# Optimization experiments

Hardware: AMD Instinct MI355X
Metric: run time of the kernel (lower is better)

Reference implementation:

```python
import jax, jax.numpy as jnp
import numpy as np
from jax import lax

HID = 256   # hidden_size
NN = 25     # n_nodes
T = 50      # seq_len
FIN = 16    # obs_length + 4
AS = 8      # action_space
HEADS = 5   # gat_head_num
E = 100     # edges per graph
B = 256     # batch


def setup_inputs() -> dict:
    key = jax.random.key(0)
    ks = jax.random.split(key, 32)
    s = 0.02
    def p(i, shape):
        return jax.random.normal(ks[i], shape, jnp.float32) * s
    return {
        "obs": jax.random.normal(ks[0], (B, NN, T, FIN), jnp.float32),
        "obs_map": jax.random.normal(ks[1], (B, 3, 84, 84), jnp.float32),
        "edges": jax.random.randint(ks[2], (B, 2, E), 0, NN),
        "edges_feature": jax.random.normal(ks[3], (B, E, 4), jnp.float32),
        "mlp_w": p(4, (FIN, HID)), "mlp_b": p(5, (HID,)),
        "c1_w": p(6, (32, 3, 8, 8)), "c1_b": p(7, (32,)),
        "c2_w": p(8, (64, 32, 4, 4)), "c2_b": p(9, (64,)),
        "c3_w": p(10, (64, 64, 3, 3)), "c3_b": p(11, (64,)),
        "fc_w": p(12, (3136, HID)), "fc_b": p(13, (HID,)),
        "gru_wih": p(14, (3 * HID, HID)), "gru_whh": p(15, (3 * HID, HID)),
        "gru_bih": p(16, (3 * HID,)), "gru_bhh": p(17, (3 * HID,)),
        "gat_wl": p(18, (HID, HEADS * HID)), "gat_bl": p(19, (HEADS * HID,)),
        "gat_wr": p(20, (HID, HEADS * HID)), "gat_br": p(21, (HEADS * HID,)),
        "gat_att": p(22, (HEADS, HID)), "gat_bias": p(23, (HID,)),
        "hid_w": p(24, (HID, HID)), "hid_b": p(25, (HID,)),
        "out_w": p(26, (HID, 1)), "out_b": p(27, (1,)),
        "adv_w": p(28, (HID, AS)), "adv_b": p(29, (AS,)),
    }


def _cnn(x, c1w, c1b, c2w, c2b, c3w, c3b, fcw, fcb):
    # Nature-CNN encoder: [B,3,84,84] -> [B,HID]
    dn = ('NCHW', 'OIHW', 'NCHW')
    h = jax.nn.relu(lax.conv_general_dilated(x, c1w, (4, 4), 'VALID', dimension_numbers=dn) + c1b[None, :, None, None])
    h = jax.nn.relu(lax.conv_general_dilated(h, c2w, (2, 2), 'VALID', dimension_numbers=dn) + c2b[None, :, None, None])
    h = jax.nn.relu(lax.conv_general_dilated(h, c3w, (1, 1), 'VALID', dimension_numbers=dn) + c3b[None, :, None, None])
    h = h.reshape(h.shape[0], -1)  # [B, 64*7*7]
    return jax.nn.relu(h @ fcw + fcb)


def _gru_last(x, wih, whh, bih, bhh):
    # torch nn.GRU (batch_first), return final hidden state [B,H]
    H = whh.shape[1]
    xg = x @ wih.T + bih  # precompute input gates [B,T,3H]
    def step(h, xg_t):
        hg = h @ whh.T + bhh
        xr, xz, xn = jnp.split(xg_t, 3, axis=-1)
        hr, hz, hn = jnp.split(hg, 3, axis=-1)
        r = jax.nn.sigmoid(xr + hr)
        z = jax.nn.sigmoid(xz + hz)
        n = jnp.tanh(xn + r * hn)
        return (1.0 - z) * n + z * h, None
    h0 = jnp.zeros((x.shape[0], H), x.dtype)
    hT, _ = lax.scan(step, h0, jnp.swapaxes(xg, 0, 1))
    return hT


def _gat(x, ei, wl, bl, wr, br, att, gbias):
    # GATv2Conv (concat=False): one graph, x [N,H], ei [2,E'] incl. self loops
    n = x.shape[0]
    heads, ch = att.shape
    src, dst = ei[0], ei[1]
    gl = (x @ wl + bl).reshape(n, heads, ch)
    gr = (x @ wr + br).reshape(n, heads, ch)
    e = jax.nn.leaky_relu(gl[src] + gr[dst], 0.2)          # [E',H,C]
    score = jnp.einsum('ehc,hc->eh', e, att)               # [E',H]
    m = jax.ops.segment_max(score, dst, num_segments=n)
    ex = jnp.exp(score - m[dst])
    den = jax.ops.segment_sum(ex, dst, num_segments=n)
    alpha = ex / den[dst]                                   # softmax per dst node
    out = jax.ops.segment_sum(alpha[:, :, None] * gl[src], dst, num_segments=n)
    return out.mean(axis=1) + gbias, alpha                  # mean over heads (concat=False)


def reference(obs, obs_map, edges, edges_feature, mlp_w, mlp_b, c1_w, c1_b, c2_w, c2_b, c3_w, c3_b, fc_w, fc_b, gru_wih, gru_whh, gru_bih, gru_bhh, gat_wl, gat_bl, gat_wr, gat_br, gat_att, gat_bias, hid_w, hid_b, out_w, out_b, adv_w, adv_b):
    bsz, n = obs.shape[0], obs.shape[1]
    n_edges = edges.shape[2]
    target_emb = _cnn(obs_map, c1_w, c1_b, c2_w, c2_b, c3_w, c3_b, fc_w, fc_b)[:, None, :]
    nbrs = obs[:, 1:].reshape(bsz * (n - 1), obs.shape[2], obs.shape[3])
    nbrs_emb = jax.nn.relu(nbrs @ mlp_w + mlp_b)            # MLP_rnn (Linear+ReLU)
    nbrs_h = _gru_last(nbrs_emb, gru_wih, gru_whh, gru_bih, gru_bhh).reshape(bsz, n - 1, -1)
    node_emb = jnp.concatenate([target_emb, nbrs_h], axis=1)  # [B,N,HID]
    loops = jnp.broadcast_to(jnp.arange(n)[None, None, :], (bsz, 2, n))
    ei = jnp.concatenate([edges, loops], axis=2)            # PyG add_self_loops (appended)
    gat_out, alpha = jax.vmap(lambda xg, eg: _gat(xg, eg, gat_wl, gat_bl, gat_wr, gat_br, gat_att, gat_bias))(node_emb, ei)
    att_w = alpha[:, : n_edges + 1].mean(axis=-1)           # matches att_weights[:-n_nodes+1].mean(axis=1)
    h = jax.nn.relu(gat_out[:, 0] @ hid_w + hid_b)          # only node-0 feature used
    v = h @ out_w + out_b
    adv = h @ adv_w + adv_b
    q = v + (adv - adv.mean(axis=-1, keepdims=True))        # dueling head
    return q, att_w
```

## Files before the change

### kernel.cpp

```cpp
#include <hip/hip_runtime.h>
#include <cstdint>

typedef __attribute__((ext_vector_type(8))) __bf16 bf16x8;
typedef __attribute__((ext_vector_type(4))) float f32x4;
typedef __attribute__((ext_vector_type(4))) unsigned int uint4v;
typedef __attribute__((ext_vector_type(2))) unsigned int uint2v;
typedef __attribute__((ext_vector_type(4))) float float4v;
typedef __attribute__((ext_vector_type(2))) long long2v;

__device__ __forceinline__ unsigned short f2bf(float x){
  union { float f; unsigned u; } v; v.f = x;
  unsigned r = v.u + 0x7FFFu + ((v.u >> 16) & 1u);
  return (unsigned short)(r >> 16);
}
__device__ __forceinline__ float bf2f(unsigned short h){
  union { unsigned u; float f; } v; v.u = ((unsigned)h) << 16;
  return v.f;
}
__device__ __forceinline__ float bflo(unsigned u){
  union { unsigned x; float f; } v; v.x = u << 16; return v.f;
}
__device__ __forceinline__ float bfhi(unsigned u){
  union { unsigned x; float f; } v; v.x = u & 0xFFFF0000u; return v.f;
}
__device__ __forceinline__ f32x4 MFMA16(bf16x8 a, bf16x8 b, f32x4 c){
  return __builtin_amdgcn_mfma_f32_16x16x32_bf16(a, b, c, 0, 0, 0);
}
__device__ __forceinline__ f32x4 MFMA8(long a, long b, f32x4 c){
  return __builtin_amdgcn_mfma_f32_16x16x32_fp8_fp8(a, b, c, 0, 0, 0);
}
__device__ __forceinline__ unsigned char f2fp8(float x){
  int p = __builtin_amdgcn_cvt_pk_fp8_f32(x, x, 0, false);
  return (unsigned char)(p & 0xFF);
}

__global__ __launch_bounds__(256) void prep_k(
    const float* __restrict__ wih, const float* __restrict__ whh,
    const float* __restrict__ bl, const float* __restrict__ br,
    const float* __restrict__ mlpw,
    const float* __restrict__ c2w, const float* __restrict__ c3w,
    const float* __restrict__ fcw, const float* __restrict__ wl, const float* __restrict__ wr,
    unsigned char* __restrict__ wfrag8, unsigned short* __restrict__ mlpfrag,
    float* __restrict__ blbr,
    unsigned short* __restrict__ c2wb, unsigned short* __restrict__ c3wb,
    unsigned short* __restrict__ fcwT, unsigned short* __restrict__ wlrT){
  __shared__ float tile[64][65];
  int bid = blockIdx.x, t = threadIdx.x;
  if (bid < 1850){
    int i = bid*256 + t;
    if (i < 393216){
      int b16 = i & 15;
      int l   = (i >> 4) & 63;
      int chunk = i >> 10;
      int wkp = chunk / 6;
      int mg  = chunk - 6*wkp;
      int w = wkp >> 2, kkp = wkp & 3;
      int ks = b16 >> 3, e = b16 & 7;
      int kk = kkp*2 + ks;
      int mat = mg / 3, g = mg - 3*(mg/3);
      int n = g*256 + w*16 + (l & 15);
      int k = kk*32 + (l >> 4)*8 + e;
      float v = 16.f * (mat ? whh[n*256 + k] : wih[n*256 + k]);
      wfrag8[i] = f2fp8(v);
      return;
    }
    i -= 393216;
    if (i < 8192){
      int w = i >> 9;
      int r4 = i & 511;
      int l = r4 >> 3, e = r4 & 7;
      int n = w*16 + (l & 15);
      int k = (l >> 4)*8 + e;
      mlpfrag[i] = (k < 16) ? f2bf(mlpw[k*256 + n]) : (unsigned short)0;
      return;
    }
    i -= 8192;
    if (i < 2560){
      blbr[i] = (i < 1280) ? bl[i] : br[i-1280];
      return;
    }
    i -= 2560;
    if (i < 32768){ c2wb[i] = f2bf(c2w[i]); return; }
    i -= 32768;
    if (i < 36864){ c3wb[i] = f2bf(c3w[i]); }
    return;
  }
  if (bid < 2046){
    int tb = bid - 1850;
    int ti = tb >> 2, tj = tb & 3;
    for (int idx = t; idx < 4096; idx += 256){
      int r = idx >> 6, c = idx & 63;
      tile[r][c] = fcw[(size_t)(ti*64 + r)*256 + tj*64 + c];
    }
    __syncthreads();
    for (int idx = t; idx < 4096; idx += 256){
      int r = idx >> 6, c = idx & 63;
      fcwT[(size_t)(tj*64 + r)*3136 + ti*64 + c] = f2bf(tile[c][r]);
    }
    return;
  }
  {
    int tb = bid - 2046;
    int m = tb / 80; int rem = tb - m*80;
    int tk = rem / 20, tn = rem - tk*20;
    const float* src = m ? wr : wl;
    for (int idx = t; idx < 4096; idx += 256){
      int r = idx >> 6, c = idx & 63;
      tile[r][c] = src[(size_t)(tk*64 + r)*1280 + tn*64 + c];
    }
    __syncthreads();
    for (int idx = t; idx < 4096; idx += 256){
      int r = idx >> 6, c = idx & 63;
      wlrT[(size_t)(m*1280 + tn*64 + r)*256 + tk*64 + c] = f2bf(tile[c][r]);
    }
  }
}

__global__ __launch_bounds__(1024) void conv23_k(const unsigned short* __restrict__ c1o,
              const unsigned short* __restrict__ c2wb, const float* __restrict__ c2b,
              const unsigned short* __restrict__ c3wb, const float* __restrict__ c3b,
              unsigned short* __restrict__ c3o){
  __shared__ __align__(16) char cs[102016];
  unsigned short* in_s = (unsigned short*)cs;
  unsigned short* w2s  = (unsigned short*)(cs + 25600);
  float* b2            = (float*)(cs + 91136);
  unsigned short* c2s  = (unsigned short*)(cs + 91392);
  unsigned short* w3s  = (unsigned short*)cs;
  float* b3            = (float*)(cs + 101760);
  int b = blockIdx.x, t = threadIdx.x;
  int q = t >> 8, t2 = t & 255;
  for (int idx = t; idx < 12800; idx += 1024) in_s[idx] = c1o[(size_t)b*12800 + idx];
  for (int idx = t; idx < 32768; idx += 1024) w2s[idx] = c2wb[idx];
  if (t < 64) b2[t] = c2b[t];
  if (t >= 64 && t < 128) b3[t-64] = c3b[t-64];
  __syncthreads();
  for (int p = t2; p < 432; p += 256){
    int ocl = p / 27; int rem = p - ocl*27;
    int oy = rem / 3, og = rem - oy*3;
    int oc = q*16 + ocl;
    float a0=b2[oc],a1=b2[oc],a2=b2[oc];
    #pragma unroll 4
    for (int ic=0;ic<32;ic++){
      #pragma unroll
      for (int ky=0;ky<4;ky++){
        const unsigned short* row = &in_s[(ic*20 + oy*2+ky)*20 + og*6];
        float s[8];
        #pragma unroll
        for (int cc=0;cc<8;cc++) s[cc]=bf2f(row[cc]);
        const unsigned short* wp = &w2s[((oc*32+ic)*4+ky)*4];
        #pragma unroll
        for (int kx=0;kx<4;kx++){
          float wv = bf2f(wp[kx]);
          a0 += s[kx]*wv; a1 += s[2+kx]*wv; a2 += s[4+kx]*wv;
        }
      }
    }
    int ob = (oc*9 + oy)*9 + og*3;
    c2s[ob+0]=f2bf(fmaxf(a0,0.f)); c2s[ob+1]=f2bf(fmaxf(a1,0.f)); c2s[ob+2]=f2bf(fmaxf(a2,0.f));
  }
  __syncthreads();
  for (int idx = t; idx < 36864; idx += 1024) w3s[idx] = c3wb[idx];
  __syncthreads();
  for (int p = t2; p < 224; p += 256){
    int ocl = p / 14; int rem = p - ocl*14;
    int oy = rem >> 1, og = rem & 1;
    int ox0 = og*4; int nx = og ? 3 : 4;
    int oc = q*16 + ocl;
    float a[4]; a[0]=a[1]=a[2]=a[3]=b3[oc];
    for (int ic=0;ic<64;ic++){
      #pragma unroll
      for (int ky=0;ky<3;ky++){
        const unsigned short* row = &c2s[(ic*9 + oy+ky)*9 + ox0];
        float s[6];
        #pragma unroll
        for (int cc=0;cc<6;cc++) s[cc] = (ox0+cc < 9) ? bf2f(row[cc]) : 0.f;
        const unsigned short* wp = &w3s[((oc*64+ic)*3+ky)*3];
        #pragma unroll
        for (int kx=0;kx<3;kx++){
          float wv = bf2f(wp[kx]);
          #pragma unroll
          for (int jj=0;jj<4;jj++) a[jj] += s[jj+kx]*wv;
        }
      }
    }
    size_t ob = (size_t)b*3136 + oc*49 + oy*7 + ox0;
    #pragma unroll
    for (int jj=0;jj<4;jj++) if (jj < nx) c3o[ob+jj] = f2bf(fmaxf(a[jj],0.f));
  }
}

__global__ __launch_bounds__(256) void gemm_k(const unsigned short* __restrict__ A,
              const unsigned short* __restrict__ B, const float* __restrict__ bias,
              unsigned short* __restrict__ C, int K, int ldc, int rowmul, int relu, int Nblk){
  __shared__ __align__(16) unsigned short As[64*32];
  __shared__ __align__(16) unsigned short Bs[64*32];
  int bid = blockIdx.x;
  int nb = bid % Nblk, mb = bid / Nblk;
  int t = threadIdx.x;
  int w = t >> 6, l = t & 63, lr = l & 15, lh = l >> 4;
  int sr = t >> 2, sq = t & 3;
  f32x4 acc[4];
  #pragma unroll
  for (int i=0;i<4;i++) acc[i] = (f32x4){0.f,0.f,0.f,0.f};
  int nkk = K >> 5;
  const size_t a_row = (size_t)(mb*64 + sr)*K;
  const size_t b_row = (size_t)(nb*64 + sr)*K;
  for (int kk=0;kk<nkk;kk++){
    uint4v av = *(const uint4v*)&A[a_row + kk*32 + sq*8];
    uint4v bv = *(const uint4v*)&B[b_row + kk*32 + sq*8];
    __syncthreads();
    *(uint4v*)((char*)As + ((sr*64 + sq*16) ^ ((sr&3)<<4))) = av;
    *(uint4v*)((char*)Bs + ((sr*64 + sq*16) ^ ((sr&3)<<4))) = bv;
    __syncthreads();
    int brow = w*16 + lr;
    bf16x8 bfr = *(const bf16x8*)((char*)Bs + ((brow*64 + lh*16) ^ ((brow&3)<<4)));
    #pragma unroll
    for (int mt=0;mt<4;mt++){
      int arow = mt*16 + lr;
      bf16x8 afr = *(const bf16x8*)((char*)As + ((arow*64 + lh*16) ^ ((arow&3)<<4)));
      acc[mt] = MFMA16(afr, bfr, acc[mt]);
    }
  }
  int col = nb*64 + w*16 + lr;
  float bn = bias[col];
  #pragma unroll
  for (int mt=0;mt<4;mt++){
    #pragma unroll
    for (int r=0;r<4;r++){
      int row = mb*64 + mt*16 + lh*4 + r;
      float v = acc[mt][r] + bn;
      if (relu) v = fmaxf(v, 0.f);
      C[(size_t)row*rowmul*ldc + col] = f2bf(v);
    }
  }
}

__global__ __launch_bounds__(256) void gemm_fc_k(const unsigned short* __restrict__ A,
              const unsigned short* __restrict__ B, float* __restrict__ P){
  __shared__ __align__(16) unsigned short As[64*32];
  __shared__ __align__(16) unsigned short Bs[64*32];
  int bid = blockIdx.x;
  int s = bid % 7, tile = bid / 7;
  int nb = tile & 3, mb = tile >> 2;
  int t = threadIdx.x;
  int w = t >> 6, l = t & 63, lr = l & 15, lh = l >> 4;
  int sr = t >> 2, sq = t & 3;
  f32x4 acc[4];
  #pragma unroll
  for (int i=0;i<4;i++) acc[i] = (f32x4){0.f,0.f,0.f,0.f};
  const int K = 3136;
  const size_t a_row = (size_t)(mb*64 + sr)*K;
  const size_t b_row = (size_t)(nb*64 + sr)*K;
  for (int kk = s*14; kk < s*14 + 14; kk++){
    uint4v av = *(const uint4v*)&A[a_row + kk*32 + sq*8];
    uint4v bv = *(const uint4v*)&B[b_row + kk*32 + sq*8];
    __syncthreads();
    *(uint4v*)((char*)As + ((sr*64 + sq*16) ^ ((sr&3)<<4))) = av;
    *(uint4v*)((char*)Bs + ((sr*64 + sq*16) ^ ((sr&3)<<4))) = bv;
    __syncthreads();
    int brow = w*16 + lr;
    bf16x8 bfr = *(const bf16x8*)((char*)Bs + ((brow*64 + lh*16) ^ ((brow&3)<<4)));
    #pragma unroll
    for (int mt=0;mt<4;mt++){
      int arow = mt*16 + lr;
      bf16x8 afr = *(const bf16x8*)((char*)As + ((arow*64 + lh*16) ^ ((arow&3)<<4)));
      acc[mt] = MFMA16(afr, bfr, acc[mt]);
    }
  }
  int col = nb*64 + w*16 + lr;
  #pragma unroll
  for (int mt=0;mt<4;mt++){
    #pragma unroll
    for (int r=0;r<4;r++){
      int row = mb*64 + mt*16 + lh*4 + r;
      P[(size_t)s*65536 + row*256 + col] = acc[mt][r];
    }
  }
}

__global__ __launch_bounds__(256) void fc_red_k(const float* __restrict__ P,
              const float* __restrict__ fcb, unsigned short* __restrict__ nemb){
  int idx = blockIdx.x*256 + threadIdx.x;
  int row = idx >> 8, col = idx & 255;
  float sum = fcb[col];
  #pragma unroll
  for (int k=0;k<7;k++) sum += P[k*65536 + idx];
  nemb[(size_t)row*25*256 + col] = f2bf(fmaxf(sum, 0.f));
}

__global__ __launch_bounds__(1024, 4)
void gruconv_k(const float* __restrict__ obs,
              const unsigned char* __restrict__ wfrag8,
              const unsigned short* __restrict__ mlpfrag,
              const float* __restrict__ mlpb,
              const float* __restrict__ bih, const float* __restrict__ bhh,
              unsigned short* __restrict__ nemb,
              const float* __restrict__ cin, const float* __restrict__ c1w,
              const float* __restrict__ c1b, unsigned short* __restrict__ c1o){
  __shared__ __align__(16) char smem[121984];

  const int t = threadIdx.x, blk = blockIdx.x;

  if (blk >= 192){
    float* in_s = (float*)smem;
    float* w_s  = (float*)(smem + 96768);
    float* b_s  = (float*)(smem + 121344);
    int b = blk - 192;
    int q = t >> 8, t2 = t & 255;
    float* inq = in_s + q*6048;
    for (int idx = t2; idx < 3*24*84; idx += 256){
      int ic = idx / (24*84); int rem = idx - ic*(24*84);
      int iy = rem / 84, ix = rem - iy*84;
      inq[idx] = cin[((size_t)(b*3+ic)*84 + (q*20 + iy))*84 + ix];
    }
    for (int idx = t; idx < 32*192; idx += 1024) w_s[idx] = c1w[idx];
    if (t < 32) b_s[t] = c1b[t];
    __syncthreads();
    for (int p = t2; p < 800; p += 256){
      int oc = p / 25; int rem = p - oc*25;
      int oy = rem / 5, og = rem - oy*5;
      float a0=b_s[oc],a1=b_s[oc],a2=b_s[oc],a3=b_s[oc];
      #pragma unroll
      for (int ic=0;ic<3;ic++){
        #pragma unroll
        for (int ky=0;ky<8;ky++){
          const float* row = &inq[(ic*24 + oy*4+ky)*84 + og*16];
          float s[20];
          #pragma unroll
          for (int cc=0;cc<20;cc++) s[cc]=row[cc];
          const float* wp = &w_s[(oc*3 + ic)*64 + ky*8];
          #pragma unroll
          for (int kx=0;kx<8;kx++){
            float wv = wp[kx];
            a0 += s[kx]*wv; a1 += s[4+kx]*wv; a2 += s[8+kx]*wv; a3 += s[12+kx]*wv;
          }
        }
      }
      size_t ob = ((size_t)(b*32+oc)*20 + (q*5+oy))*20 + og*4;
      c1o[ob+0]=f2bf(fmaxf(a0,0.f)); c1o[ob+1]=f2bf(fmaxf(a1,0.f));
      c1o[ob+2]=f2bf(fmaxf(a2,0.f)); c1o[ob+3]=f2bf(fmaxf(a3,0.f));
    }
    return;
  }

  unsigned short* obsA = (unsigned short*)smem;
  unsigned char* e8_0 = (unsigned char*)(smem + 2048);
  unsigned char* e8_1 = (unsigned char*)(smem + 10240);
  unsigned char* h8   = (unsigned char*)(smem + 18432);

  obsA[t & 1023] = 0;
  for (int j = t; j < 8192; j += 1024) h8[j] = 0;

  const int w = t >> 6, l = t & 63, lr = l & 15, lh = l >> 4;
  const int jcol = w*16 + lr;
  const float bR  = bih[jcol]     + bhh[jcol];
  const float bZ  = bih[256+jcol] + bhh[256+jcol];
  const float bXN = bih[512+jcol];
  const float bHN = bhh[512+jcol];
  const float bMb = mlpb[jcol];
  const bf16x8 bMLP = *(const bf16x8*)(mlpfrag + w*512 + l*8);

  const unsigned char* wb8 = wfrag8 + w*24576 + l*16;

  const int srow = t >> 2, sk4 = t & 3;
  int rrS = blk*32 + srow; int bS = rrS/24, ndS = 1 + (rrS - bS*24);
  const float* obase4 = obs + (size_t)(bS*25 + ndS)*800 + sk4*4;
  const int obyte = (srow*64 + sk4*8) ^ ((srow&3)<<4);

  const int a8off = lr*256 + lh*8;
  const int xr8 = lr << 3;
  const int o16 = lh*16;
  const int oa0b = (lr*64 + o16) ^ ((lr&3)<<4);
  const int oa1b = ((16+lr)*64 + o16) ^ ((lr&3)<<4);
  const int hw0 = jcol;
  const float S = 1.f/256.f;

  f32x4 hs0 = (f32x4){0.f,0.f,0.f,0.f};
  f32x4 hs1 = (f32x4){0.f,0.f,0.f,0.f};

#define EMB_COMPUTE(DST) { \
  f32x4 e0 = (f32x4){0.f,0.f,0.f,0.f}, e1 = (f32x4){0.f,0.f,0.f,0.f}; \
  bf16x8 oa0 = *(const bf16x8*)((char*)obsA + oa0b); \
  bf16x8 oa1 = *(const bf16x8*)((char*)obsA + oa1b); \
  e0 = MFMA16(oa0, bMLP, e0); \
  e1 = MFMA16(oa1, bMLP, e1); \
  _Pragma("unroll") \
  for (int r=0;r<4;r++){ \
    int m = lh*4 + r; \
    (DST)[(m*256 + hw0) ^ ((m&15)<<3)] = f2fp8(fmaxf(e0[r] + bMb, 0.f)*16.f); \
    int m2 = m + 16; \
    (DST)[(m2*256 + hw0) ^ ((m2&15)<<3)] = f2fp8(fmaxf(e1[r] + bMb, 0.f)*16.f); \
  } }

  __syncthreads();
  if (t < 128){
    float4v ov = *(const float4v*)(obase4);
    uint2v pk;
    pk[0] = (unsigned)f2bf(ov[0]) | ((unsigned)f2bf(ov[1]) << 16);
    pk[1] = (unsigned)f2bf(ov[2]) | ((unsigned)f2bf(ov[3]) << 16);
    *(uint2v*)((char*)obsA + obyte) = pk;
  }
  __syncthreads();
  EMB_COMPUTE(e8_0)
  __syncthreads();

  for (int step=0; step<50; step++){
    const unsigned char* ebuf = (step & 1) ? e8_1 : e8_0;
    unsigned char* nbuf = (step & 1) ? e8_0 : e8_1;
    const bool stg = (t < 128) && (step < 49);
    float4v ov;
    if (stg) ov = *(const float4v*)(obase4 + (size_t)(step+1)*16);

    f32x4 aR0=(f32x4){0,0,0,0}, aR1=(f32x4){0,0,0,0};
    f32x4 aZ0=(f32x4){0,0,0,0}, aZ1=(f32x4){0,0,0,0};
    f32x4 aN0=(f32x4){0,0,0,0}, aN1=(f32x4){0,0,0,0};
    f32x4 aM0=(f32x4){0,0,0,0}, aM1=(f32x4){0,0,0,0};
    __builtin_amdgcn_s_setprio(1);
    #pragma unroll 2
    for (int kkp=0;kkp<4;kkp++){
      const unsigned char* wk8 = wb8 + kkp*6144;
      long2v wIR = *(const long2v*)(wk8);
      long2v wIZ = *(const long2v*)(wk8 + 1024);
      long2v wIN = *(const long2v*)(wk8 + 2048);
      long2v wHR = *(const long2v*)(wk8 + 3072);
      long2v wHZ = *(const long2v*)(wk8 + 4096);
      long2v wHN = *(const long2v*)(wk8 + 5120);
      {
        int kk = kkp*2;
        int ab = a8off + kk*32;
        long eA0 = *(const long*)(ebuf + (ab ^ xr8));
        long eA1 = *(const long*)(ebuf + ((ab + 4096) ^ xr8));
        long hA0 = *(const long*)(h8 + (ab ^ xr8));
        long hA1 = *(const long*)(h8 + ((ab + 4096) ^ xr8));
        aR0 = MFMA8(eA0, wIR[0], aR0);  aR0 = MFMA8(hA0, wHR[0], aR0);
        aR1 = MFMA8(eA1, wIR[0], aR1);  aR1 = MFMA8(hA1, wHR[0], aR1);
        aZ0 = MFMA8(eA0, wIZ[0], aZ0);  aZ0 = MFMA8(hA0, wHZ[0], aZ0);
        aZ1 = MFMA8(eA1, wIZ[0], aZ1);  aZ1 = MFMA8(hA1, wHZ[0], aZ1);
        aN0 = MFMA8(eA0, wIN[0], aN0);  aN1 = MFMA8(eA1, wIN[0], aN1);
        aM0 = MFMA8(hA0, wHN[0], aM0);  aM1 = MFMA8(hA1, wHN[0], aM1);
      }
      {
        int kk = kkp*2 + 1;
        int ab = a8off + kk*32;
        long eA0 = *(const long*)(ebuf + (ab ^ xr8));
        long eA1 = *(const long*)(ebuf + ((ab + 4096) ^ xr8));
        long hA0 = *(const long*)(h8 + (ab ^ xr8));
        long hA1 = *(const long*)(h8 + ((ab + 4096) ^ xr8));
        aR0 = MFMA8(eA0, wIR[1], aR0);  aR0 = MFMA8(hA0, wHR[1], aR0);
        aR1 = MFMA8(eA1, wIR[1], aR1);  aR1 = MFMA8(hA1, wHR[1], aR1);
        aZ0 = MFMA8(eA0, wIZ[1], aZ0);  aZ0 = MFMA8(hA0, wHZ[1], aZ0);
        aZ1 = MFMA8(eA1, wIZ[1], aZ1);  aZ1 = MFMA8(hA1, wHZ[1], aZ1);
        aN0 = MFMA8(eA0, wIN[1], aN0);  aN1 = MFMA8(eA1, wIN[1], aN1);
        aM0 = MFMA8(hA0, wHN[1], aM0);  aM1 = MFMA8(hA1, wHN[1], aM1);
      }
    }
    __builtin_amdgcn_s_setprio(0);
    if (stg){
      uint2v pk;
      pk[0] = (unsigned)f2bf(ov[0]) | ((unsigned)f2bf(ov[1]) << 16);
      pk[1] = (unsigned)f2bf(ov[2]) | ((unsigned)f2bf(ov[3]) << 16);
      *(uint2v*)((char*)obsA + obyte) = pk;
    }
    __syncthreads();
    if (step < 49){
      EMB_COMPUTE(nbuf)
    }
    #pragma unroll
    for (int mt=0;mt<2;mt++){
      f32x4 vR = mt ? aR1 : aR0;
      f32x4 vZ = mt ? aZ1 : aZ0;
      f32x4 vN = mt ? aN1 : aN0;
      f32x4 vM = mt ? aM1 : aM0;
      #pragma unroll
      for (int r=0;r<4;r++){
        float rp = vR[r]*S + bR;
        float zp = vZ[r]*S + bZ;
        float xn = vN[r]*S + bXN;
        float hn = vM[r]*S + bHN;
        float rg = 1.f/(1.f + __expf(-rp));
        float zg = 1.f/(1.f + __expf(-zp));
        float arg = xn + rg*hn;
        float e2 = __expf(2.f*arg);
        float nv = (e2 - 1.f)/(e2 + 1.f);
        float hold = mt ? hs1[r] : hs0[r];
        float hnew = (1.f - zg)*nv + zg*hold;
        if (mt) hs1[r] = hnew; else hs0[r] = hnew;
        int m = mt*16 + lh*4 + r;
        h8[(m*256 + hw0) ^ ((m&15)<<3)] = f2fp8(hnew*16.f);
        if (step == 49){
          int rr = blk*32 + m; int b = rr/24; int nd = 1 + (rr - b*24);
          nemb[(size_t)(b*25+nd)*256 + jcol] = f2bf(hnew);
        }
      }
    }
    __syncthreads();
  }
#undef EMB_COMPUTE
}

__global__ __launch_bounds__(1024) void gat_k(const int* __restrict__ edges,
              const unsigned short* __restrict__ glgr,
              const float* __restrict__ att, const float* __restrict__ gbias,
              const float* __restrict__ hidw, const float* __restrict__ hidb,
              const float* __restrict__ outw, const float* __restrict__ outb,
              const float* __restrict__ advw, const float* __restrict__ advb,
              float* __restrict__ out){
  __shared__ int src_s[125], dst_s[125];
  __shared__ __align__(16) float att_s[1280];
  __shared__ float sc[125][5], al[125][5];
  __shared__ float mx[25][5], dn[25][5];
  __shared__ float g0p[4][256];
  __shared__ float hp[4][256];
  __shared__ float g0[256], hh[256];
  __shared__ float adv_s[8], v_s;
  __shared__ int e0[125]; __shared__ int ne0;

  int b = blockIdx.x, t = threadIdx.x;
  int qq = t >> 8, t2 = t & 255;
  if (t < 100){ src_s[t] = edges[b*200 + t]; dst_s[t] = edges[b*200 + 100 + t]; }
  else if (t < 125){ src_s[t] = t - 100; dst_s[t] = t - 100; }
  for (int j = t; j < 1280; j += 1024) att_s[j] = att[j];
  __syncthreads();
  if (t == 0){ int c = 0; for (int e=0;e<125;e++) if (dst_s[e]==0) e0[c++]=e; ne0 = c; }
  const unsigned short* gbase = glgr + (size_t)b*25*2560;
  if (t < 625){
    int e = t/5, h = t - 5*(t/5);
    const unsigned short* glp = gbase + src_s[e]*2560 + h*256;
    const unsigned short* grp = gbase + dst_s[e]*2560 + 1280 + h*256;
    const float* ap = &att_s[h*256];
    float acc = 0.f;
    #pragma unroll 4
    for (int c=0;c<256;c+=8){
      uint4v gu = *(const uint4v*)&glp[c];
      uint4v ru = *(const uint4v*)&grp[c];
      #pragma unroll
      for (int q=0;q<4;q++){
        float s0 = bflo(gu[q]) + bflo(ru[q]);
        float s1 = bfhi(gu[q]) + bfhi(ru[q]);
        s0 = (s0 > 0.f) ? s0 : 0.2f*s0;
        s1 = (s1 > 0.f) ? s1 : 0.2f*s1;
        acc += s0*ap[c+2*q] + s1*ap[c+2*q+1];
      }
    }
    sc[e][h] = acc;
  }
  __syncthreads();
  if (t < 125){
    int j = t/5, h = t - 5*(t/5);
    float m = -1e30f;
    for (int e=0;e<125;e++) if (dst_s[e]==j) m = fmaxf(m, sc[e][h]);
    float d = 0.f;
    for (int e=0;e<125;e++) if (dst_s[e]==j) d += __expf(sc[e][h]-m);
    mx[j][h] = m; dn[j][h] = d;
  }
  __syncthreads();
  if (t < 625){
    int e = t/5, h = t - 5*(t/5);
    int dd = dst_s[e];
    al[e][h] = __expf(sc[e][h] - mx[dd][h]) / dn[dd][h];
  }
  __syncthreads();
  if (t < 101){
    out[2048 + b*101 + t] = (al[t][0]+al[t][1]+al[t][2]+al[t][3]+al[t][4])*0.2f;
  }
  {
    float acc = 0.f;
    for (int x=qq; x<ne0; x+=4){
      int e = e0[x]; int s = src_s[e];
      const unsigned short* glp = gbase + s*2560 + t2;
      #pragma unroll
      for (int h=0;h<5;h++) acc += al[e][h]*bf2f(glp[h*256]);
    }
    g0p[qq][t2] = acc;
  }
  __syncthreads();
  if (t < 256){
    g0[t] = (g0p[0][t]+g0p[1][t]+g0p[2][t]+g0p[3][t])*0.2f + gbias[t];
  }
  __syncthreads();
  {
    float acc = 0.f;
    int k0 = qq*64;
    for (int k=k0;k<k0+64;k++) acc += g0[k]*hidw[k*256+t2];
    hp[qq][t2] = acc;
  }
  __syncthreads();
  if (t < 256){
    hh[t] = fmaxf(hidb[t] + hp[0][t]+hp[1][t]+hp[2][t]+hp[3][t], 0.f);
  }
  __syncthreads();
  if (t < 8){
    float acc = advb[t];
    for (int k=0;k<256;k++) acc += hh[k]*advw[k*8+t];
    adv_s[t] = acc;
  } else if (t == 8){
    float acc = outb[0];
    for (int k=0;k<256;k++) acc += hh[k]*outw[k];
    v_s = acc;
  }
  __syncthreads();
  if (t < 8){
    float m = adv_s[0]+adv_s[1]+adv_s[2]+adv_s[3]+adv_s[4]+adv_s[5]+adv_s[6]+adv_s[7];
    out[b*8+t] = v_s + adv_s[t] - m*0.125f;
  }
}

extern "C" void kernel_launch(void* const* d_in, const int* in_sizes, int n_in,
                              void* d_out, int out_size, void* d_ws, size_t ws_size,
                              hipStream_t stream){
  const float* obs     = (const float*)d_in[0];
  const float* obs_map = (const float*)d_in[1];
  const int*   edges   = (const int*)d_in[2];
  const float* mlp_w = (const float*)d_in[4];
  const float* mlp_b = (const float*)d_in[5];
  const float* c1w = (const float*)d_in[6];  const float* c1b = (const float*)d_in[7];
  const float* c2w = (const float*)d_in[8];  const float* c2b = (const float*)d_in[9];
  const float* c3w = (const float*)d_in[10]; const float* c3b = (const float*)d_in[11];
  const float* fcw = (const float*)d_in[12]; const float* fcb = (const float*)d_in[13];
  const float* wih = (const float*)d_in[14]; const float* whh = (const float*)d_in[15];
  const float* bih = (const float*)d_in[16]; const float* bhh = (const float*)d_in[17];
  const float* gwl = (const float*)d_in[18]; const float* gbl = (const float*)d_in[19];
  const float* gwr = (const float*)d_in[20]; const float* gbr = (const float*)d_in[21];
  const float* gatt = (const float*)d_in[22]; const float* gbias = (const float*)d_in[23];
  const float* hidw = (const float*)d_in[24]; const float* hidb = (const float*)d_in[25];
  const float* outw = (const float*)d_in[26]; const float* outb = (const float*)d_in[27];
  const float* advw = (const float*)d_in[28]; const float* advb = (const float*)d_in[29];
  float* out = (float*)d_out;
  char* ws = (char*)d_ws;

  unsigned short* c1o  = (unsigned short*)(ws + 0);
  unsigned short* c3o  = (unsigned short*)(ws + 6553600);
  float*          fcpart = (float*)(ws + 16000000);
  unsigned short* glgr = (unsigned short*)(ws + 0);
  size_t o = 32768000;
  unsigned short* nemb    = (unsigned short*)(ws + o); o += 3276800;
  unsigned char*  wfrag8  = (unsigned char*)(ws + o);  o += 393216;
  unsigned short* mlpfrag = (unsigned short*)(ws + o); o += 16384;
  unsigned short* wlrT    = (unsigned short*)(ws + o); o += 1310720;
  unsigned short* fcwT    = (unsigned short*)(ws + o); o += 1605632;
  float* blbr             = (float*)(ws + o); o += 10240;
  unsigned short* c2wb    = (unsigned short*)(ws + o); o += 65536;
  unsigned short* c3wb    = (unsigned short*)(ws + o); o += 73728;

  prep_k<<<2206, 256, 0, stream>>>(wih, whh, gbl, gbr, mlp_w, c2w, c3w, fcw, gwl, gwr,
                                   wfrag8, mlpfrag, blbr, c2wb, c3wb, fcwT, wlrT);
  gruconv_k<<<448, 1024, 0, stream>>>(obs, wfrag8, mlpfrag, mlp_b, bih, bhh, nemb,
                                      obs_map, c1w, c1b, c1o);
  conv23_k<<<256, 1024, 0, stream>>>(c1o, c2wb, c2b, c3wb, c3b, c3o);
  gemm_fc_k<<<112, 256, 0, stream>>>(c3o, fcwT, fcpart);
  fc_red_k<<<256, 256, 0, stream>>>(fcpart, fcb, nemb);
  gemm_k<<<4000, 256, 0, stream>>>(nemb, wlrT, blbr, glgr, 256, 2560, 1, 0, 40);
  gat_k<<<256, 1024, 0, stream>>>(edges, glgr, gatt, gbias, hidw, hidb, outw, outb, advw, advb, out);
}
```

Baseline: 730.7 us.

## Double-buffer obs and hidden state to drop one barrier per GRU step

Adds a second buffer for both the staged observation tile and the fp8 hidden state, and prefetches observations two steps ahead. Reads and writes now go to different buffers within a step, so the mid-step __syncthreads between the MFMA accumulation and the embedding/gate write-back is removed, leaving one barrier per step instead of two. The cost is more shared memory per block (an extra obs buffer and an extra 8 KB hidden buffer) and more complex buffer indexing. The larger LDS footprint could reduce occupancy if it exceeds limits.

```diff
diff --git a/kernel.cpp b/kernel.cpp
--- a/kernel.cpp
+++ b/kernel.cpp
@@ -343,13 +343,16 @@
     return;
   }
 
-  unsigned short* obsA = (unsigned short*)smem;
-  unsigned char* e8_0 = (unsigned char*)(smem + 2048);
-  unsigned char* e8_1 = (unsigned char*)(smem + 10240);
-  unsigned char* h8   = (unsigned char*)(smem + 18432);
-
-  obsA[t & 1023] = 0;
-  for (int j = t; j < 8192; j += 1024) h8[j] = 0;
+  unsigned short* obsA0 = (unsigned short*)smem;
+  unsigned short* obsA1 = (unsigned short*)(smem + 2048);
+  unsigned char* e8_0 = (unsigned char*)(smem + 4096);
+  unsigned char* e8_1 = (unsigned char*)(smem + 12288);
+  unsigned char* h8_0 = (unsigned char*)(smem + 20480);
+  unsigned char* h8_1 = (unsigned char*)(smem + 28672);
+
+  obsA0[t & 1023] = 0;
+  obsA1[t & 1023] = 0;
+  for (int j = t; j < 8192; j += 1024) h8_0[j] = 0;
 
   const int w = t >> 6, l = t & 63, lr = l & 15, lh = l >> 4;
   const int jcol = w*16 + lr;
@@ -378,10 +381,17 @@
   f32x4 hs0 = (f32x4){0.f,0.f,0.f,0.f};
   f32x4 hs1 = (f32x4){0.f,0.f,0.f,0.f};
 
-#define EMB_COMPUTE(DST) { \
+#define STAGE_OBS(DST, STEP) { \
+  float4v ov = *(const float4v*)(obase4 + (size_t)(STEP)*16); \
+  uint2v pk; \
+  pk[0] = (unsigned)f2bf(ov[0]) | ((unsigned)f2bf(ov[1]) << 16); \
+  pk[1] = (unsigned)f2bf(ov[2]) | ((unsigned)f2bf(ov[3]) << 16); \
+  *(uint2v*)((char*)(DST) + obyte) = pk; }
+
+#define EMB_COMPUTE(SRC, DST) { \
   f32x4 e0 = (f32x4){0.f,0.f,0.f,0.f}, e1 = (f32x4){0.f,0.f,0.f,0.f}; \
-  bf16x8 oa0 = *(const bf16x8*)((char*)obsA + oa0b); \
-  bf16x8 oa1 = *(const bf16x8*)((char*)obsA + oa1b); \
+  bf16x8 oa0 = *(const bf16x8*)((char*)(SRC) + oa0b); \
+  bf16x8 oa1 = *(const bf16x8*)((char*)(SRC) + oa1b); \
   e0 = MFMA16(oa0, bMLP, e0); \
   e1 = MFMA16(oa1, bMLP, e1); \
   _Pragma("unroll") \
@@ -394,22 +404,24 @@
 
   __syncthreads();
   if (t < 128){
-    float4v ov = *(const float4v*)(obase4);
-    uint2v pk;
-    pk[0] = (unsigned)f2bf(ov[0]) | ((unsigned)f2bf(ov[1]) << 16);
-    pk[1] = (unsigned)f2bf(ov[2]) | ((unsigned)f2bf(ov[3]) << 16);
-    *(uint2v*)((char*)obsA + obyte) = pk;
-  }
-  __syncthreads();
-  EMB_COMPUTE(e8_0)
+    STAGE_OBS(obsA0, 0)
+    STAGE_OBS(obsA1, 1)
+  }
+  __syncthreads();
+  EMB_COMPUTE(obsA0, e8_0)
   __syncthreads();
 
   for (int step=0; step<50; step++){
-    const unsigned char* ebuf = (step & 1) ? e8_1 : e8_0;
-    unsigned char* nbuf = (step & 1) ? e8_0 : e8_1;
-    const bool stg = (t < 128) && (step < 49);
+    const int c = step & 1;
+    const unsigned char* ebuf = c ? e8_1 : e8_0;
+    const unsigned char* hbuf = c ? h8_1 : h8_0;
+    unsigned char* enew = c ? e8_0 : e8_1;
+    unsigned char* hnewb = c ? h8_0 : h8_1;
+    const unsigned short* obsRd = c ? obsA0 : obsA1;
+    unsigned short* obsWr = c ? obsA1 : obsA0;
+    const bool stg = (t < 128) && (step < 48);
     float4v ov;
-    if (stg) ov = *(const float4v*)(obase4 + (size_t)(step+1)*16);
+    if (stg) ov = *(const float4v*)(obase4 + (size_t)(step+2)*16);
 
     f32x4 aR0=(f32x4){0,0,0,0}, aR1=(f32x4){0,0,0,0};
     f32x4 aZ0=(f32x4){0,0,0,0}, aZ1=(f32x4){0,0,0,0};
@@ -430,8 +442,8 @@
         int ab = a8off + kk*32;
         long eA0 = *(const long*)(ebuf + (ab ^ xr8));
         long eA1 = *(const long*)(ebuf + ((ab + 4096) ^ xr8));
-        long hA0 = *(const long*)(h8 + (ab ^ xr8));
-        long hA1 = *(const long*)(h8 + ((ab + 4096) ^ xr8));
+        long hA0 = *(const long*)(hbuf + (ab ^ xr8));
+        long hA1 = *(const long*)(hbuf + ((ab + 4096) ^ xr8));
         aR0 = MFMA8(eA0, wIR[0], aR0);  aR0 = MFMA8(hA0, wHR[0], aR0);
         aR1 = MFMA8(eA1, wIR[0], aR1);  aR1 = MFMA8(hA1, wHR[0], aR1);
         aZ0 = MFMA8(eA0, wIZ[0], aZ0);  aZ0 = MFMA8(hA0, wHZ[0], aZ0);
@@ -444,8 +456,8 @@
         int ab = a8off + kk*32;
         long eA0 = *(const long*)(ebuf + (ab ^ xr8));
         long eA1 = *(const long*)(ebuf + ((ab + 4096) ^ xr8));
-        long hA0 = *(const long*)(h8 + (ab ^ xr8));
-        long hA1 = *(const long*)(h8 + ((ab + 4096) ^ xr8));
+        long hA0 = *(const long*)(hbuf + (ab ^ xr8));
+        long hA1 = *(const long*)(hbuf + ((ab + 4096) ^ xr8));
         aR0 = MFMA8(eA0, wIR[1], aR0);  aR0 = MFMA8(hA0, wHR[1], aR0);
         aR1 = MFMA8(eA1, wIR[1], aR1);  aR1 = MFMA8(hA1, wHR[1], aR1);
         aZ0 = MFMA8(eA0, wIZ[1], aZ0);  aZ0 = MFMA8(hA0, wHZ[1], aZ0);
@@ -459,11 +471,10 @@
       uint2v pk;
       pk[0] = (unsigned)f2bf(ov[0]) | ((unsigned)f2bf(ov[1]) << 16);
       pk[1] = (unsigned)f2bf(ov[2]) | ((unsigned)f2bf(ov[3]) << 16);
-      *(uint2v*)((char*)obsA + obyte) = pk;
-    }
-    __syncthreads();
+      *(uint2v*)((char*)obsWr + obyte) = pk;
+    }
     if (step < 49){
-      EMB_COMPUTE(nbuf)
+      EMB_COMPUTE(obsRd, enew)
     }
     #pragma unroll
     for (int mt=0;mt<2;mt++){
@@ -486,7 +497,7 @@
         float hnew = (1.f - zg)*nv + zg*hold;
         if (mt) hs1[r] = hnew; else hs0[r] = hnew;
         int m = mt*16 + lh*4 + r;
-        h8[(m*256 + hw0) ^ ((m&15)<<3)] = f2fp8(hnew*16.f);
+        hnewb[(m*256 + hw0) ^ ((m&15)<<3)] = f2fp8(hnew*16.f);
         if (step == 49){
           int rr = blk*32 + m; int b = rr/24; int nd = 1 + (rr - b*24);
           nemb[(size_t)(b*25+nd)*256 + jcol] = f2bf(hnew);
@@ -495,6 +506,7 @@
     }
     __syncthreads();
   }
+#undef STAGE_OBS
 #undef EMB_COMPUTE
 }
 
```

Result: faster. 690.8 us (-5.5%).
